# Optimization experiments

Measured on AMD Instinct MI355X. Metric: run time of the kernel, lower is better.

Reference implementation:

```python
import jax, jax.numpy as jnp
import numpy as np

DIM = 1024

def setup_inputs() -> dict:
    key = jax.random.key(0)
    k1, k2, k3, k4, k5 = jax.random.split(key, 5)
    x = jax.random.normal(k1, (8, 2048, DIM), dtype=jnp.float32)
    # nn.Linear-style params: W is [out, in], b is [out]
    s = 1.0 / np.sqrt(DIM)
    W1 = jax.random.uniform(k2, (DIM, DIM), jnp.float32, -s, s)
    b1 = jax.random.uniform(k3, (DIM,), jnp.float32, -s, s)
    W2 = jax.random.uniform(k4, (DIM, DIM), jnp.float32, -s, s)
    b2 = jax.random.uniform(k5, (DIM,), jnp.float32, -s, s)
    return {"x": x, "W1": W1, "b1": b1, "W2": W2, "b2": b2}

def reference(x, W1, b1, W2, b2):
    # NOTE: original module reuses linear_1 for BOTH V and Q (linear_3 unused)
    V = x @ W1.T + b1                      # [B,S,D]
    K = x @ W2.T + b2                      # [B,S,D]
    Q = x @ W1.T + b1                      # [B,S,D]
    scale = 1.0 / jnp.sqrt(jnp.float32(x.shape[-1]))
    scores = jnp.einsum('bkd,bqd->bkq', K, Q) * scale  # K @ Q^T, [B,S,S]
    attn = jax.nn.softmax(scores, axis=-1)
    out = jnp.einsum('bkq,bqd->bkd', attn, V)
    return out
```

## Files before the change

kernel.cpp:

```cpp
#include <hip/hip_runtime.h>
#include <hip/hip_fp16.h>
#include <cstdint>
#include <cstddef>

#define DIMK 1024
#define NBATCH 8
#define SEQ 2048

typedef _Float16 half8 __attribute__((ext_vector_type(8)));
typedef _Float16 half4_t __attribute__((ext_vector_type(4)));
typedef float float4_t __attribute__((ext_vector_type(4)));

__device__ __forceinline__ void ld16_to_lds(const _Float16* g, _Float16* l) {
  __builtin_amdgcn_global_load_lds((const __attribute__((address_space(1))) void*)g,
                                   (__attribute__((address_space(3))) void*)l, 16, 0, 0);
}

template <int SA, int SB, int KDIM>
__device__ __forceinline__ void mfma_core(const _Float16* __restrict__ Ag,
                                          const _Float16* __restrict__ Bg,
                                          _Float16* As, _Float16* Bs,
                                          float4_t (&acc)[4][4],
                                          int lane, int wave) {
  const int col = lane & 15, quad = lane >> 4;
  const int wm = (wave >> 1) * 64, wn = (wave & 1) * 64;
  const int lr = lane >> 3;
  const int lg = (lane & 7) ^ lr;
  for (int k0 = 0; k0 < KDIM; k0 += 64) {
#pragma unroll
    for (int c = 0; c < 4; ++c) {
      const int r0 = (wave + 4 * c) * 8;
      const int r = r0 + lr;
      ld16_to_lds(Ag + (size_t)r * SA + k0 + lg * 8, &As[r0 * 64]);
      ld16_to_lds(Bg + (size_t)r * SB + k0 + lg * 8, &Bs[r0 * 64]);
    }
    __syncthreads();
#pragma unroll
    for (int kk = 0; kk < 2; ++kk) {
      half8 af[4], bf[4];
#pragma unroll
      for (int mi = 0; mi < 4; ++mi) {
        int row = wm + mi * 16 + col;
        af[mi] = *(const half8*)(&As[(row << 6) + ((((kk << 2) + quad) ^ (row & 7)) << 3)]);
      }
#pragma unroll
      for (int nj = 0; nj < 4; ++nj) {
        int row = wn + nj * 16 + col;
        bf[nj] = *(const half8*)(&Bs[(row << 6) + ((((kk << 2) + quad) ^ (row & 7)) << 3)]);
      }
#pragma unroll
      for (int mi = 0; mi < 4; ++mi)
#pragma unroll
        for (int nj = 0; nj < 4; ++nj)
          acc[mi][nj] = __builtin_amdgcn_mfma_f32_16x16x32_f16(af[mi], bf[nj], acc[mi][nj], 0, 0, 0);
    }
    __syncthreads();
  }
}

__global__ __launch_bounds__(256) void cvt_kernel(const float* __restrict__ in,
                                                  _Float16* __restrict__ out, int n4) {
  int i = blockIdx.x * 256 + threadIdx.x;
  if (i >= n4) return;
  float4_t v = ((const float4_t*)in)[i];
  half4_t h;
  h[0] = (_Float16)v[0]; h[1] = (_Float16)v[1];
  h[2] = (_Float16)v[2]; h[3] = (_Float16)v[3];
  ((half4_t*)out)[i] = h;
}

__global__ __launch_bounds__(256) void zero_kernel(float* __restrict__ p, int n) {
  int i = blockIdx.x * 256 + threadIdx.x;
  if (i < n) p[i] = 0.0f;
}

__global__ __launch_bounds__(256) void gemm_vk_kernel(const _Float16* __restrict__ xh,
                                                      const _Float16* __restrict__ Wcat,
                                                      const float* __restrict__ b1,
                                                      const float* __restrict__ b2,
                                                      _Float16* __restrict__ Vbuf,
                                                      _Float16* __restrict__ Kbuf) {
  __shared__ _Float16 As[128 * 64];
  __shared__ _Float16 Bs[128 * 64];
  const int tid = threadIdx.x, lane = tid & 63, wave = tid >> 6;
  const int bm = blockIdx.x, bn = blockIdx.y;
  float4_t acc[4][4] = {};
  mfma_core<DIMK, DIMK, DIMK>(xh + (size_t)bm * 128 * DIMK,
                              Wcat + (size_t)bn * 128 * DIMK, As, Bs, acc, lane, wave);
  const int col = lane & 15, quad = lane >> 4;
  const int wm = (wave >> 1) * 64, wn = (wave & 1) * 64;
  _Float16* dst = (bn < 8) ? Vbuf : Kbuf;
  const float* bias = (bn < 8) ? b1 : b2;
  const int nbase = (bn & 7) * 128;
#pragma unroll
  for (int nj = 0; nj < 4; ++nj) {
    int gcol = nbase + wn + nj * 16 + col;
    float bv = bias[gcol];
#pragma unroll
    for (int mi = 0; mi < 4; ++mi) {
#pragma unroll
      for (int r = 0; r < 4; ++r) {
        int grow = bm * 128 + wm + mi * 16 + quad * 4 + r;
        dst[(size_t)grow * DIMK + gcol] = (_Float16)(acc[mi][nj][r] + bv);
      }
    }
  }
}

__global__ __launch_bounds__(256) void gemm_scores_kernel(const _Float16* __restrict__ Kb,
                                                          const _Float16* __restrict__ Vb,
                                                          _Float16* __restrict__ P,
                                                          float* __restrict__ rsum) {
  __shared__ _Float16 As[128 * 64];
  __shared__ _Float16 Bs[128 * 64];
  const int tid = threadIdx.x, lane = tid & 63, wave = tid >> 6;
  const int bm = blockIdx.x, bn = blockIdx.y, b = blockIdx.z;
  float4_t acc[4][4] = {};
  mfma_core<DIMK, DIMK, DIMK>(Kb + (size_t)(b * SEQ + bm * 128) * DIMK,
                              Vb + (size_t)(b * SEQ + bn * 128) * DIMK, As, Bs, acc, lane, wave);
  const int col = lane & 15, quad = lane >> 4;
  const int wm = (wave >> 1) * 64, wn = (wave & 1) * 64;
  _Float16* Pb = P + (size_t)b * SEQ * SEQ;
  float* rs = rsum + b * SEQ;
#pragma unroll
  for (int mi = 0; mi < 4; ++mi) {
#pragma unroll
    for (int r = 0; r < 4; ++r) {
      int grow = bm * 128 + wm + mi * 16 + quad * 4 + r;
      float sum = 0.0f;
#pragma unroll
      for (int nj = 0; nj < 4; ++nj) {
        int gcol = bn * 128 + wn + nj * 16 + col;
        float p = __expf(acc[mi][nj][r] * 0.03125f);
        Pb[(size_t)grow * 2048 + gcol] = (_Float16)p;
        sum += p;
      }
      sum += __shfl_xor(sum, 1, 64);
      sum += __shfl_xor(sum, 2, 64);
      sum += __shfl_xor(sum, 4, 64);
      sum += __shfl_xor(sum, 8, 64);
      if (col == 0) atomicAdd(&rs[grow], sum);
    }
  }
}

__global__ __launch_bounds__(256) void transpose_v_kernel(const _Float16* __restrict__ V,
                                                          _Float16* __restrict__ Vt) {
  __shared__ _Float16 t[64][72];
  const int tid = threadIdx.x;
  const int q0 = blockIdx.x * 64, d0 = blockIdx.y * 64, b = blockIdx.z;
  for (int i = tid; i < 512; i += 256) {
    int q = i >> 3, g = i & 7;
    *(half8*)(&t[q][g * 8]) = *(const half8*)(V + (size_t)(b * SEQ + q0 + q) * DIMK + d0 + g * 8);
  }
  __syncthreads();
  for (int i = tid; i < 512; i += 256) {
    int d = i >> 3, g = i & 7;
    half8 v;
#pragma unroll
    for (int j = 0; j < 8; j++) v[j] = t[g * 8 + j][d];
    *(half8*)(Vt + (size_t)b * DIMK * SEQ + (size_t)(d0 + d) * SEQ + q0 + g * 8) = v;
  }
}

__global__ __launch_bounds__(256) void gemm_out_kernel(const _Float16* __restrict__ P,
                                                       const _Float16* __restrict__ Vt,
                                                       const float* __restrict__ rsum,
                                                       float* __restrict__ out) {
  __shared__ _Float16 As[128 * 64];
  __shared__ _Float16 Bs[128 * 64];
  const int tid = threadIdx.x, lane = tid & 63, wave = tid >> 6;
  const int bm = blockIdx.x, bn = blockIdx.y, b = blockIdx.z;
  float4_t acc[4][4] = {};
  mfma_core<SEQ, SEQ, SEQ>(P + (size_t)(b * SEQ + bm * 128) * SEQ,
                           Vt + (size_t)(b * DIMK + bn * 128) * SEQ, As, Bs, acc, lane, wave);
  const int col = lane & 15, quad = lane >> 4;
  const int wm = (wave >> 1) * 64, wn = (wave & 1) * 64;
  const float* rs = rsum + b * SEQ + bm * 128;
#pragma unroll
  for (int nj = 0; nj < 4; ++nj) {
    int gcol = bn * 128 + wn + nj * 16 + col;
#pragma unroll
    for (int mi = 0; mi < 4; ++mi) {
#pragma unroll
      for (int r = 0; r < 4; ++r) {
        int lrow = wm + mi * 16 + quad * 4 + r;
        out[((size_t)(b * SEQ) + bm * 128 + lrow) * DIMK + gcol] = acc[mi][nj][r] / rs[lrow];
      }
    }
  }
}

extern "C" void kernel_launch(void* const* d_in, const int* in_sizes, int n_in,
                              void* d_out, int out_size, void* d_ws, size_t ws_size,
                              hipStream_t stream) {
  const float* x  = (const float*)d_in[0];
  const float* W1 = (const float*)d_in[1];
  const float* b1 = (const float*)d_in[2];
  const float* W2 = (const float*)d_in[3];
  const float* b2 = (const float*)d_in[4];
  float* out = (float*)d_out;

  char* ws = (char*)d_ws;
  _Float16* xh   = (_Float16*)(ws);
  _Float16* Pbuf = (_Float16*)(ws);
  _Float16* Vbuf = (_Float16*)(ws + 67108864);
  _Float16* Kbuf = (_Float16*)(ws + 100663296);
  _Float16* Vt   = Kbuf;
  _Float16* Wcat = (_Float16*)(ws + 134217728);
  float*    rsum = (float*)(ws + 138412032);

  cvt_kernel<<<16384, 256, 0, stream>>>(x, xh, 4194304);
  cvt_kernel<<<1024, 256, 0, stream>>>(W1, Wcat, 262144);
  cvt_kernel<<<1024, 256, 0, stream>>>(W2, Wcat + 1048576, 262144);
  zero_kernel<<<64, 256, 0, stream>>>(rsum, 16384);

  gemm_vk_kernel<<<dim3(128, 16), 256, 0, stream>>>(xh, Wcat, b1, b2, Vbuf, Kbuf);
  gemm_scores_kernel<<<dim3(16, 16, 8), 256, 0, stream>>>(Kbuf, Vbuf, Pbuf, rsum);
  transpose_v_kernel<<<dim3(32, 16, 8), 256, 0, stream>>>(Vbuf, Vt);
  gemm_out_kernel<<<dim3(16, 8, 8), 256, 0, stream>>>(Pbuf, Vt, rsum, out);
}
```

Before: 406.4 us.

## Fuse prep kernels, remap tiles per XCD, use reciprocal in output epilogue

Merges the three conversion launches and the rsum zeroing into one prep kernel to cut launch overhead. Remaps block indices in the scores and output GEMMs so blocks landing on the same XCD share A/B row panels, aiming for better L2 reuse. Replaces the per-element division in the output epilogue with one hardware reciprocal per row and reorders the loops. The reciprocal is approximate and may differ slightly in the last bits.

```diff
diff --git a/kernel.cpp b/kernel.cpp
--- a/kernel.cpp
+++ b/kernel.cpp
@@ -58,20 +58,31 @@
   }
 }
 
-__global__ __launch_bounds__(256) void cvt_kernel(const float* __restrict__ in,
-                                                  _Float16* __restrict__ out, int n4) {
+__global__ __launch_bounds__(256) void prep_kernel(const float* __restrict__ x,
+                                                   const float* __restrict__ W1,
+                                                   const float* __restrict__ W2,
+                                                   _Float16* __restrict__ xh,
+                                                   _Float16* __restrict__ Wcat,
+                                                   float* __restrict__ rsum) {
   int i = blockIdx.x * 256 + threadIdx.x;
-  if (i >= n4) return;
-  float4_t v = ((const float4_t*)in)[i];
-  half4_t h;
-  h[0] = (_Float16)v[0]; h[1] = (_Float16)v[1];
-  h[2] = (_Float16)v[2]; h[3] = (_Float16)v[3];
-  ((half4_t*)out)[i] = h;
-}
-
-__global__ __launch_bounds__(256) void zero_kernel(float* __restrict__ p, int n) {
-  int i = blockIdx.x * 256 + threadIdx.x;
-  if (i < n) p[i] = 0.0f;
+  if (i < 4194304) {
+    float4_t v = ((const float4_t*)x)[i];
+    half4_t h; h[0]=(_Float16)v[0]; h[1]=(_Float16)v[1]; h[2]=(_Float16)v[2]; h[3]=(_Float16)v[3];
+    ((half4_t*)xh)[i] = h;
+  } else if (i < 4456448) {
+    int j = i - 4194304;
+    float4_t v = ((const float4_t*)W1)[j];
+    half4_t h; h[0]=(_Float16)v[0]; h[1]=(_Float16)v[1]; h[2]=(_Float16)v[2]; h[3]=(_Float16)v[3];
+    ((half4_t*)Wcat)[j] = h;
+  } else if (i < 4718592) {
+    int j = i - 4456448;
+    float4_t v = ((const float4_t*)W2)[j];
+    half4_t h; h[0]=(_Float16)v[0]; h[1]=(_Float16)v[1]; h[2]=(_Float16)v[2]; h[3]=(_Float16)v[3];
+    ((half4_t*)(Wcat + 1048576))[j] = h;
+  } else if (i < 4722688) {
+    float4_t z = {0.0f, 0.0f, 0.0f, 0.0f};
+    ((float4_t*)rsum)[i - 4718592] = z;
+  }
 }
 
 __global__ __launch_bounds__(256) void gemm_vk_kernel(const _Float16* __restrict__ xh,
@@ -114,7 +125,11 @@
   __shared__ _Float16 As[128 * 64];
   __shared__ _Float16 Bs[128 * 64];
   const int tid = threadIdx.x, lane = tid & 63, wave = tid >> 6;
-  const int bm = blockIdx.x, bn = blockIdx.y, b = blockIdx.z;
+  const int flat = blockIdx.x + (blockIdx.y << 4);
+  const int xcd = flat & 7, loc = flat >> 3;
+  const int bm = ((xcd & 3) << 2) + (loc & 3);
+  const int bn = ((xcd >> 2) << 3) + (loc >> 2);
+  const int b = blockIdx.z;
   float4_t acc[4][4] = {};
   mfma_core<DIMK, DIMK, DIMK>(Kb + (size_t)(b * SEQ + bm * 128) * DIMK,
                               Vb + (size_t)(b * SEQ + bn * 128) * DIMK, As, Bs, acc, lane, wave);
@@ -170,7 +185,11 @@
   __shared__ _Float16 As[128 * 64];
   __shared__ _Float16 Bs[128 * 64];
   const int tid = threadIdx.x, lane = tid & 63, wave = tid >> 6;
-  const int bm = blockIdx.x, bn = blockIdx.y, b = blockIdx.z;
+  const int flat = blockIdx.x + (blockIdx.y << 4);
+  const int xcd = flat & 7, loc = flat >> 3;
+  const int bm = ((xcd & 3) << 2) + (loc & 3);
+  const int bn = ((xcd >> 2) << 2) + (loc >> 2);
+  const int b = blockIdx.z;
   float4_t acc[4][4] = {};
   mfma_core<SEQ, SEQ, SEQ>(P + (size_t)(b * SEQ + bm * 128) * SEQ,
                            Vt + (size_t)(b * DIMK + bn * 128) * SEQ, As, Bs, acc, lane, wave);
@@ -178,14 +197,15 @@
   const int wm = (wave >> 1) * 64, wn = (wave & 1) * 64;
   const float* rs = rsum + b * SEQ + bm * 128;
 #pragma unroll
-  for (int nj = 0; nj < 4; ++nj) {
-    int gcol = bn * 128 + wn + nj * 16 + col;
-#pragma unroll
-    for (int mi = 0; mi < 4; ++mi) {
-#pragma unroll
-      for (int r = 0; r < 4; ++r) {
-        int lrow = wm + mi * 16 + quad * 4 + r;
-        out[((size_t)(b * SEQ) + bm * 128 + lrow) * DIMK + gcol] = acc[mi][nj][r] / rs[lrow];
+  for (int mi = 0; mi < 4; ++mi) {
+#pragma unroll
+    for (int r = 0; r < 4; ++r) {
+      int lrow = wm + mi * 16 + quad * 4 + r;
+      float inv = __builtin_amdgcn_rcpf(rs[lrow]);
+#pragma unroll
+      for (int nj = 0; nj < 4; ++nj) {
+        int gcol = bn * 128 + wn + nj * 16 + col;
+        out[((size_t)(b * SEQ) + bm * 128 + lrow) * DIMK + gcol] = acc[mi][nj][r] * inv;
       }
     }
   }
@@ -210,10 +230,7 @@
   _Float16* Wcat = (_Float16*)(ws + 134217728);
   float*    rsum = (float*)(ws + 138412032);
 
-  cvt_kernel<<<16384, 256, 0, stream>>>(x, xh, 4194304);
-  cvt_kernel<<<1024, 256, 0, stream>>>(W1, Wcat, 262144);
-  cvt_kernel<<<1024, 256, 0, stream>>>(W2, Wcat + 1048576, 262144);
-  zero_kernel<<<64, 256, 0, stream>>>(rsum, 16384);
+  prep_kernel<<<18448, 256, 0, stream>>>(x, W1, W2, xh, Wcat, rsum);
 
   gemm_vk_kernel<<<dim3(128, 16), 256, 0, stream>>>(xh, Wcat, b1, b2, Vbuf, Kbuf);
   gemm_scores_kernel<<<dim3(16, 16, 8), 256, 0, stream>>>(Kbuf, Vbuf, Pbuf, rsum);
```

Measured after the change: 410.0 us. No clear change (+0.9%).
